# Kernel tuning notes

Measured on AMD Instinct MI355X. Metric: run time of the kernel, lower is better.

Reference implementation:

```python
import jax, jax.numpy as jnp
import numpy as np

B, D = 8192, 128


def setup_inputs() -> dict:
    key = jax.random.key(0)
    ks = jax.random.split(key, 7)
    s = 1.0 / np.sqrt(D)  # torch Linear default init scale
    x = jax.random.normal(ks[0], (B, D), jnp.float32)
    W1 = jax.random.uniform(ks[1], (D, D), jnp.float32, -s, s)
    b1 = jax.random.uniform(ks[2], (D,), jnp.float32, -s, s)
    Wmu = jax.random.uniform(ks[3], (D, D), jnp.float32, -s, s)
    bmu = jax.random.uniform(ks[4], (D,), jnp.float32, -s, s)
    Wls = jax.random.uniform(ks[5], (D, D), jnp.float32, -s, s)
    bls = jax.random.uniform(ks[6], (D,), jnp.float32, -s, s)
    return {"x": x, "W1": W1, "b1": b1, "Wmu": Wmu, "bmu": bmu, "Wls": Wls, "bls": bls}


def reference(x, W1, b1, Wmu, bmu, Wls, bls):
    d = x.shape[1]
    mask = jnp.tril(jnp.ones((d, d), x.dtype), -1)  # strict lower triangular, as in MaskedLinear
    W1m = W1 * mask
    Wmum = Wmu * mask
    Wlsm = Wls * mask

    def step(carry, i):
        z, ldj = carry
        h = jax.nn.relu(z @ W1m.T + b1)          # [B, D] hidden (MaskedLinear + ReLU)
        # only column i of mu/logs is consumed each step -> use weight row i
        mu_i = h @ Wmum[i] + bmu[i]              # [B]
        logs_i = h @ Wlsm[i] + bls[i]            # [B]
        z = z.at[:, i].set(mu_i + x[:, i] * jnp.exp(logs_i))
        return (z, ldj + logs_i), None

    z0 = jnp.zeros_like(x)
    ldj0 = jnp.zeros(x.shape[0], x.dtype)
    (z, ldj), _ = jax.lax.scan(step, (z0, ldj0), jnp.arange(d))
    return z, ldj
```

## Files before the change

kernel.cpp:

```cpp
#include <hip/hip_runtime.h>
#include <stdint.h>

#define D 128
#define LOG2E 1.4426950408889634f
#define LN2 0.6931471805599453f

typedef float f2 __attribute__((ext_vector_type(2)));
typedef float f4 __attribute__((ext_vector_type(4)));

__device__ __forceinline__ uint16_t f2bf(float f) {
  uint32_t u = __float_as_uint(f);
  u += 0x7fffu + ((u >> 16) & 1u);
  return (uint16_t)(u >> 16);
}
__device__ __forceinline__ uint32_t pkbf(float a, float b) {
  return (uint32_t)f2bf(a) | ((uint32_t)f2bf(b) << 16);
}
__device__ __forceinline__ f2 unpkbf(uint32_t u) {
  f2 r;
  r.x = __uint_as_float(u << 16);
  r.y = __uint_as_float(u & 0xffff0000u);
  return r;
}
__device__ __forceinline__ float rdlane(float v, int l) {
  return __int_as_float(__builtin_amdgcn_readlane(__float_as_int(v), l));
}
__device__ __forceinline__ float exp2x(float v) {
#if __has_builtin(__builtin_amdgcn_exp2f)
  return __builtin_amdgcn_exp2f(v);
#else
  return exp2f(v);
#endif
}

#define WS_NEED (size_t)(3 * 2048 * 16)

__global__ __launch_bounds__(256)
void iaf_prep(const float* __restrict__ W1, const float* __restrict__ Wmu,
              const float* __restrict__ Wls, uint4* __restrict__ ws) {
  const int t = blockIdx.x * 256 + threadIdx.x;
  if (t >= 32 * 64) return;
  const int jb = t >> 6, l = t & 63;
  const int k0 = 2 * l, k1 = 2 * l + 1;
  uint32_t mm[4], ll[4], ww[4];
#pragma unroll
  for (int c = 0; c < 4; ++c) {
    const int j = jb * 4 + c;
    const float m0 = (j < k0) ? Wmu[k0 * D + j] : 0.f;
    const float m1 = (j < k1) ? Wmu[k1 * D + j] : 0.f;
    const float s0 = (j < k0) ? Wls[k0 * D + j] * LOG2E : 0.f;
    const float s1 = (j < k1) ? Wls[k1 * D + j] * LOG2E : 0.f;
    const float w0 = (j < k0) ? W1[k0 * D + j] : 0.f;
    const float w1_ = (j < k1) ? W1[k1 * D + j] : 0.f;
    mm[c] = pkbf(m0, m1);
    ll[c] = pkbf(s0, s1);
    ww[c] = pkbf(w0, w1_);
  }
  uint4 m4, l4, w4;
  m4.x = mm[0]; m4.y = mm[1]; m4.z = mm[2]; m4.w = mm[3];
  l4.x = ll[0]; l4.y = ll[1]; l4.z = ll[2]; l4.w = ll[3];
  w4.x = ww[0]; w4.y = ww[1]; w4.z = ww[2]; w4.w = ww[3];
  ws[t] = m4;
  ws[2048 + t] = l4;
  ws[4096 + t] = w4;
}

#define SEL(U, c) ((c) == 0 ? (U).x : (c) == 1 ? (U).y : (c) == 2 ? (U).z : (U).w)
#define E(V, c) (((c) & 1) ? (V).y : (V).x)

#define STEP(c)                                                   \
  {                                                               \
    const int Ln = jb * 2 + ((c) >> 1);                           \
    const f2 wm = unpkbf(SEL(mC, c));                             \
    const f2 wl = unpkbf(SEL(lC, c));                             \
    const f2 wv = unpkbf(SEL(wC, c));                             \
    const float h = fmaxf(E(pa, c), 0.f);                         \
    const float z = fmaf(E(xR, c), exp2x(E(pls, c)), E(pmu, c));  \
    const float sz = rdlane(z, Ln);                               \
    const float sh = rdlane(h, Ln);                               \
    f2 t;                                                         \
    t.x = sz; t.y = sz;                                           \
    pa = __builtin_elementwise_fma(t, wv, pa);                    \
    t.x = sh; t.y = sh;                                           \
    pmu = __builtin_elementwise_fma(t, wm, pmu);                  \
    pls = __builtin_elementwise_fma(t, wl, pls);                  \
  }

__global__ __launch_bounds__(1024, 8)
void iaf_main(const float* __restrict__ x, const float* __restrict__ b1,
              const float* __restrict__ bmu, const float* __restrict__ bls,
              const uint4* __restrict__ ws, float* __restrict__ out, int B) {
  __shared__ uint4 wsh[2 * 2048];

  const int tid = threadIdx.x;
#pragma unroll
  for (int k = 0; k < 4; ++k) wsh[tid + k * 1024] = ws[tid + k * 1024];

  const int lane = tid & 63;
  const int wave = tid >> 6;
  const int row = blockIdx.x * 16 + wave;
  const int l2 = lane * 2;

  const f2 xR = *(const f2*)(x + (size_t)row * D + l2);
  f2 pa = *(const f2*)(b1 + l2);
  f2 pmu = *(const f2*)(bmu + l2);
  f2 pls = *(const f2*)(bls + l2);
  pls.x *= LOG2E;
  pls.y *= LOG2E;

  const uint4* wmu4s = wsh;
  const uint4* wls4s = wsh + 2048;
  const uint4* w14g = ws + 4096;

  __syncthreads();

  uint4 mC = wmu4s[lane];
  uint4 lC = wls4s[lane];
  uint4 wC = w14g[lane];

#pragma unroll 1
  for (int jb = 0; jb < 32; ++jb) {
    const int nb = (jb + 1 < 32) ? jb + 1 : 31;
    const uint4 mN = wmu4s[nb * 64 + lane];
    const uint4 lN = wls4s[nb * 64 + lane];
    const uint4 wN = w14g[nb * 64 + lane];
    STEP(0)
    STEP(1)
    STEP(2)
    STEP(3)
    mC = mN;
    lC = lN;
    wC = wN;
  }

  f2 zf;
  zf.x = fmaf(xR.x, exp2x(pls.x), pmu.x);
  zf.y = fmaf(xR.y, exp2x(pls.y), pmu.y);
  *(f2*)(out + (size_t)row * D + l2) = zf;

  float ldj = pls.x + pls.y;
#pragma unroll
  for (int m2 = 1; m2 < 64; m2 <<= 1) ldj += __shfl_xor(ldj, m2);
  if (lane == 0) out[(size_t)B * D + row] = ldj * LN2;
}

#define FNTHR 256
#define FRPB 16
#define W1S 136
template <int CTRL>
__device__ __forceinline__ float dppmov(float v) {
  return __int_as_float(
      __builtin_amdgcn_update_dpp(0, __float_as_int(v), CTRL, 0xf, 0xf, true));
}
#define DPP_ADD(v, ctrl) (v) += dppmov<(ctrl)>((v))
__device__ __forceinline__ f2 unpk(uint32_t u) {
  f2 r;
  r.x = __uint_as_float(u << 16);
  r.y = __uint_as_float(u & 0xffff0000u);
  return r;
}
#define RED16F(v)      \
  do {                 \
    DPP_ADD(v, 0xB1);  \
    DPP_ADD(v, 0x4E);  \
    DPP_ADD(v, 0x124); \
    DPP_ADD(v, 0x128); \
  } while (0)
#define FSTEP(I, XE, ZRE, MKE, WM0, WM1, WL0, WL1)                  \
  {                                                                 \
    const float bmu_i = bmu[(I)];                                   \
    const float bls_i = bls[(I)];                                   \
    const f2 h0 = __builtin_elementwise_max(A0, (f2)0.f);           \
    const f2 h1 = __builtin_elementwise_max(A1, (f2)0.f);           \
    const f2 h2_ = __builtin_elementwise_max(A2, (f2)0.f);          \
    const f2 h3 = __builtin_elementwise_max(A3, (f2)0.f);           \
    const f2 q0 = h0 * mk0, q1 = h1 * mk1;                          \
    const f2 q2 = h2_ * mk2, q3 = h3 * mk3;                         \
    f2 am = q0 * WM0.xy;                                            \
    f2 al = q0 * WL0.xy;                                            \
    am = __builtin_elementwise_fma(q1, WM0.zw, am);                 \
    al = __builtin_elementwise_fma(q1, WL0.zw, al);                 \
    am = __builtin_elementwise_fma(q2, WM1.xy, am);                 \
    al = __builtin_elementwise_fma(q2, WL1.xy, al);                 \
    am = __builtin_elementwise_fma(q3, WM1.zw, am);                 \
    al = __builtin_elementwise_fma(q3, WL1.zw, al);                 \
    float mu_p = am.x + am.y;                                       \
    float ls_p = al.x + al.y;                                       \
    {                                                               \
      const int pfr = ((I) + 2 < D) ? (I) + 2 : D - 1;              \
      WM0 = *(const f4*)(wmup + pfr * D);                           \
      WM1 = *(const f4*)(wmup + pfr * D + 4);                       \
      WL0 = *(const f4*)(wlsp + pfr * D);                           \
      WL1 = *(const f4*)(wlsp + pfr * D + 4);                       \
    }                                                               \
    RED16F(mu_p);                                                   \
    RED16F(ls_p);                                                   \
    const float mu_t = mu_p + bmu_i;                                \
    const float ls_t = ls_p + bls_i;                                \
    const float zi = fmaf((XE), __expf(ls_t), mu_t);                \
    ldj += ls_t;                                                    \
    const uint4 wv = *(const uint4*)(w1p + (I)*W1S);                \
    if (own) {                                                      \
      ZRE = zi;                                                     \
      MKE = 1.f;                                                    \
    }                                                               \
    f2 zz;                                                          \
    zz.x = zi;                                                      \
    zz.y = zi;                                                      \
    A0 = __builtin_elementwise_fma(zz, unpk(wv.x), A0);             \
    A1 = __builtin_elementwise_fma(zz, unpk(wv.y), A1);             \
    A2 = __builtin_elementwise_fma(zz, unpk(wv.z), A2);             \
    A3 = __builtin_elementwise_fma(zz, unpk(wv.w), A3);             \
  }

__global__ __launch_bounds__(FNTHR, 2)
void iaf_fb(const float* __restrict__ x, const float* __restrict__ W1,
            const float* __restrict__ b1, const float* __restrict__ Wmu,
            const float* __restrict__ bmu, const float* __restrict__ Wls,
            const float* __restrict__ bls, float* __restrict__ out, int B) {
  __shared__ uint16_t w1c[D * W1S];
  const int tid = threadIdx.x;
  for (int idx = tid; idx < D * D; idx += FNTHR) {
    const int p = idx >> 7, q = idx & (D - 1);
    w1c[q * W1S + p] = f2bf((p > q) ? W1[idx] : 0.f);
  }
  __syncthreads();
  const int lane = tid & 63;
  const int m = lane & 15;
  const int row = blockIdx.x * FRPB + (tid >> 4);
  const float* __restrict__ xp = x + (size_t)row * D;
  const float* __restrict__ wmup = Wmu + m * 8;
  const float* __restrict__ wlsp = Wls + m * 8;
  const uint16_t* __restrict__ w1p = w1c + m * 8;
  f2 A0, A1, A2, A3;
  {
    const f4 t0 = *(const f4*)(b1 + m * 8);
    const f4 t1 = *(const f4*)(b1 + m * 8 + 4);
    A0 = t0.xy; A1 = t0.zw; A2 = t1.xy; A3 = t1.zw;
  }
  f2 mk0 = (f2)0.f, mk1 = (f2)0.f, mk2 = (f2)0.f, mk3 = (f2)0.f;
  float zr0 = 0, zr1 = 0, zr2 = 0, zr3 = 0, zr4 = 0, zr5 = 0, zr6 = 0, zr7 = 0;
  float ldj = 0.f;
  f4 wmA0 = *(const f4*)(wmup);
  f4 wmA1 = *(const f4*)(wmup + 4);
  f4 wlA0 = *(const f4*)(wlsp);
  f4 wlA1 = *(const f4*)(wlsp + 4);
  f4 wmB0 = *(const f4*)(wmup + D);
  f4 wmB1 = *(const f4*)(wmup + D + 4);
  f4 wlB0 = *(const f4*)(wlsp + D);
  f4 wlB1 = *(const f4*)(wlsp + D + 4);
  f4 x4a = *(const f4*)(xp);
  f4 x4b;
  for (int ib = 0; ib < 16; ++ib) {
    const int i0 = ib * 8;
    const bool own = (m == ib);
    x4b = *(const f4*)(xp + i0 + 4);
    FSTEP(i0 + 0, x4a.x, zr0, mk0.x, wmA0, wmA1, wlA0, wlA1);
    FSTEP(i0 + 1, x4a.y, zr1, mk0.y, wmB0, wmB1, wlB0, wlB1);
    FSTEP(i0 + 2, x4a.z, zr2, mk1.x, wmA0, wmA1, wlA0, wlA1);
    FSTEP(i0 + 3, x4a.w, zr3, mk1.y, wmB0, wmB1, wlB0, wlB1);
    {
      const int nx = (i0 + 8 < D) ? i0 + 8 : D - 4;
      x4a = *(const f4*)(xp + nx);
    }
    FSTEP(i0 + 4, x4b.x, zr4, mk2.x, wmA0, wmA1, wlA0, wlA1);
    FSTEP(i0 + 5, x4b.y, zr5, mk2.y, wmB0, wmB1, wlB0, wlB1);
    FSTEP(i0 + 6, x4b.z, zr6, mk3.x, wmA0, wmA1, wlA0, wlA1);
    FSTEP(i0 + 7, x4b.w, zr7, mk3.y, wmB0, wmB1, wlB0, wlB1);
  }
  f4 o0, o1;
  o0.x = zr0; o0.y = zr1; o0.z = zr2; o0.w = zr3;
  o1.x = zr4; o1.y = zr5; o1.z = zr6; o1.w = zr7;
  float* zo = out + (size_t)row * D + m * 8;
  *(f4*)(zo) = o0;
  *(f4*)(zo + 4) = o1;
  if (m == 0) out[(size_t)B * D + row] = ldj;
}

extern "C" void kernel_launch(void* const* d_in, const int* in_sizes, int n_in,
                              void* d_out, int out_size, void* d_ws, size_t ws_size,
                              hipStream_t stream) {
  const float* x   = (const float*)d_in[0];
  const float* W1  = (const float*)d_in[1];
  const float* b1  = (const float*)d_in[2];
  const float* Wmu = (const float*)d_in[3];
  const float* bmu = (const float*)d_in[4];
  const float* Wls = (const float*)d_in[5];
  const float* bls = (const float*)d_in[6];
  float* out = (float*)d_out;

  const int B = in_sizes[0] / D;

  if (ws_size >= WS_NEED) {
    iaf_prep<<<8, 256, 0, stream>>>(W1, Wmu, Wls, (uint4*)d_ws);
    const int grid = (B + 15) / 16;
    iaf_main<<<grid, 1024, 0, stream>>>(x, b1, bmu, bls, (const uint4*)d_ws, out, B);
  } else {
    const int grid = (B + FRPB - 1) / FRPB;
    iaf_fb<<<grid, FNTHR, 0, stream>>>(x, W1, b1, Wmu, bmu, Wls, bls, out, B);
  }
}
```

Before: 44.55 us.

## Process two batch rows per wavefront to amortize weight loads

Each wavefront now carries two independent rows through the 128-step sequential scan, reusing the same loaded and unpacked weight fragments for both. Blocks shrink from 1024 to 512 threads while still covering 16 rows, so total waves are halved. This cuts weight load and unpack cost per row and gives two independent dependency chains per wave for latency hiding. In exchange it doubles register use per thread and halves wave-level parallelism.

```diff
diff --git a/kernel.cpp b/kernel.cpp
--- a/kernel.cpp
+++ b/kernel.cpp
@@ -68,25 +68,29 @@
 #define SEL(U, c) ((c) == 0 ? (U).x : (c) == 1 ? (U).y : (c) == 2 ? (U).z : (U).w)
 #define E(V, c) (((c) & 1) ? (V).y : (V).x)
 
-#define STEP(c)                                                   \
-  {                                                               \
-    const int Ln = jb * 2 + ((c) >> 1);                           \
-    const f2 wm = unpkbf(SEL(mC, c));                             \
-    const f2 wl = unpkbf(SEL(lC, c));                             \
-    const f2 wv = unpkbf(SEL(wC, c));                             \
-    const float h = fmaxf(E(pa, c), 0.f);                         \
-    const float z = fmaf(E(xR, c), exp2x(E(pls, c)), E(pmu, c));  \
-    const float sz = rdlane(z, Ln);                               \
-    const float sh = rdlane(h, Ln);                               \
-    f2 t;                                                         \
-    t.x = sz; t.y = sz;                                           \
-    pa = __builtin_elementwise_fma(t, wv, pa);                    \
-    t.x = sh; t.y = sh;                                           \
-    pmu = __builtin_elementwise_fma(t, wm, pmu);                  \
-    pls = __builtin_elementwise_fma(t, wl, pls);                  \
-  }
-
-__global__ __launch_bounds__(1024, 8)
+#define STEP(c)                                                         \
+  {                                                                     \
+    const int Ln = jb * 2 + ((c) >> 1);                                 \
+    const f2 wm = unpkbf(SEL(mC, c));                                   \
+    const f2 wl = unpkbf(SEL(lC, c));                                   \
+    const f2 wv = unpkbf(SEL(wC, c));                                   \
+    const float hA = fmaxf(E(paA, c), 0.f);                             \
+    const float hB = fmaxf(E(paB, c), 0.f);                             \
+    const float zA = fmaf(E(xA, c), exp2x(E(plsA, c)), E(pmuA, c));     \
+    const float zB = fmaf(E(xB, c), exp2x(E(plsB, c)), E(pmuB, c));     \
+    const float szA = rdlane(zA, Ln);                                   \
+    const float shA = rdlane(hA, Ln);                                   \
+    const float szB = rdlane(zB, Ln);                                   \
+    const float shB = rdlane(hB, Ln);                                   \
+    paA = __builtin_elementwise_fma((f2)szA, wv, paA);                  \
+    pmuA = __builtin_elementwise_fma((f2)shA, wm, pmuA);                \
+    plsA = __builtin_elementwise_fma((f2)shA, wl, plsA);                \
+    paB = __builtin_elementwise_fma((f2)szB, wv, paB);                  \
+    pmuB = __builtin_elementwise_fma((f2)shB, wm, pmuB);                \
+    plsB = __builtin_elementwise_fma((f2)shB, wl, plsB);                \
+  }
+
+__global__ __launch_bounds__(512, 4)
 void iaf_main(const float* __restrict__ x, const float* __restrict__ b1,
               const float* __restrict__ bmu, const float* __restrict__ bls,
               const uint4* __restrict__ ws, float* __restrict__ out, int B) {
@@ -94,36 +98,42 @@
 
   const int tid = threadIdx.x;
 #pragma unroll
-  for (int k = 0; k < 4; ++k) wsh[tid + k * 1024] = ws[tid + k * 1024];
+  for (int k = 0; k < 8; ++k) wsh[tid + k * 512] = ws[tid + k * 512];
 
   const int lane = tid & 63;
   const int wave = tid >> 6;
-  const int row = blockIdx.x * 16 + wave;
+  const int rA = blockIdx.x * 16 + wave * 2;
+  const int rB = rA + 1;
   const int l2 = lane * 2;
 
-  const f2 xR = *(const f2*)(x + (size_t)row * D + l2);
-  f2 pa = *(const f2*)(b1 + l2);
-  f2 pmu = *(const f2*)(bmu + l2);
-  f2 pls = *(const f2*)(bls + l2);
-  pls.x *= LOG2E;
-  pls.y *= LOG2E;
-
-  const uint4* wmu4s = wsh;
-  const uint4* wls4s = wsh + 2048;
-  const uint4* w14g = ws + 4096;
+  const f2 xA = *(const f2*)(x + (size_t)rA * D + l2);
+  const f2 xB = *(const f2*)(x + (size_t)rB * D + l2);
+  f2 paA = *(const f2*)(b1 + l2);
+  f2 paB = paA;
+  f2 pmuA = *(const f2*)(bmu + l2);
+  f2 pmuB = pmuA;
+  f2 plsA = *(const f2*)(bls + l2);
+  plsA.x *= LOG2E;
+  plsA.y *= LOG2E;
+  f2 plsB = plsA;
+
+  const uint4* wmuP = wsh + lane;
+  const uint4* wlsP = wsh + 2048 + lane;
+  const uint4* w1P = ws + 4096 + lane;
 
   __syncthreads();
 
-  uint4 mC = wmu4s[lane];
-  uint4 lC = wls4s[lane];
-  uint4 wC = w14g[lane];
+  uint4 mC = wmuP[0], lC = wlsP[0], wC = w1P[0];
 
 #pragma unroll 1
   for (int jb = 0; jb < 32; ++jb) {
-    const int nb = (jb + 1 < 32) ? jb + 1 : 31;
-    const uint4 mN = wmu4s[nb * 64 + lane];
-    const uint4 lN = wls4s[nb * 64 + lane];
-    const uint4 wN = w14g[nb * 64 + lane];
+    const int adv = (jb + 1 < 32) ? 64 : 0;
+    wmuP += adv;
+    wlsP += adv;
+    w1P += adv;
+    const uint4 mN = wmuP[0];
+    const uint4 lN = wlsP[0];
+    const uint4 wN = w1P[0];
     STEP(0)
     STEP(1)
     STEP(2)
@@ -133,15 +143,25 @@
     wC = wN;
   }
 
-  f2 zf;
-  zf.x = fmaf(xR.x, exp2x(pls.x), pmu.x);
-  zf.y = fmaf(xR.y, exp2x(pls.y), pmu.y);
-  *(f2*)(out + (size_t)row * D + l2) = zf;
-
-  float ldj = pls.x + pls.y;
+  f2 zfA, zfB;
+  zfA.x = fmaf(xA.x, exp2x(plsA.x), pmuA.x);
+  zfA.y = fmaf(xA.y, exp2x(plsA.y), pmuA.y);
+  zfB.x = fmaf(xB.x, exp2x(plsB.x), pmuB.x);
+  zfB.y = fmaf(xB.y, exp2x(plsB.y), pmuB.y);
+  *(f2*)(out + (size_t)rA * D + l2) = zfA;
+  *(f2*)(out + (size_t)rB * D + l2) = zfB;
+
+  float ldjA = plsA.x + plsA.y;
+  float ldjB = plsB.x + plsB.y;
 #pragma unroll
-  for (int m2 = 1; m2 < 64; m2 <<= 1) ldj += __shfl_xor(ldj, m2);
-  if (lane == 0) out[(size_t)B * D + row] = ldj * LN2;
+  for (int m2 = 1; m2 < 64; m2 <<= 1) {
+    ldjA += __shfl_xor(ldjA, m2);
+    ldjB += __shfl_xor(ldjB, m2);
+  }
+  if (lane == 0) {
+    out[(size_t)B * D + rA] = ldjA * LN2;
+    out[(size_t)B * D + rB] = ldjB * LN2;
+  }
 }
 
 #define FNTHR 256
@@ -294,7 +314,7 @@
   if (ws_size >= WS_NEED) {
     iaf_prep<<<8, 256, 0, stream>>>(W1, Wmu, Wls, (uint4*)d_ws);
     const int grid = (B + 15) / 16;
-    iaf_main<<<grid, 1024, 0, stream>>>(x, b1, bmu, bls, (const uint4*)d_ws, out, B);
+    iaf_main<<<grid, 512, 0, stream>>>(x, b1, bmu, bls, (const uint4*)d_ws, out, B);
   } else {
     const int grid = (B + FRPB - 1) / FRPB;
     iaf_fb<<<grid, FNTHR, 0, stream>>>(x, W1, b1, Wmu, bmu, Wls, bls, out, B);
```

After: 39.22 us. 12.0% less time.
